# Performance work log

Hardware: AMD Instinct MI355X
Metric: run time of the kernel (lower is better)

## Reference

```python
import jax, jax.numpy as jnp
import numpy as np

EPS = 1e-5
NEG_SLOPE = 0.01  # torch F.leaky_relu default


def _batchnorm(h, gamma, beta):
    # BatchNorm1d in training mode: batch stats over node dim, biased variance
    mu = jnp.mean(h, axis=0)
    var = jnp.mean((h - mu) ** 2, axis=0)
    return gamma * (h - mu) * jax.lax.rsqrt(var + EPS) + beta


def setup_inputs() -> dict:
    N, E, H, ED = 16384, 524288, 128, 16
    key = jax.random.key(0)
    ks = jax.random.split(key, 12)
    s = 1.0 / np.sqrt(H)
    return {
        "x": jax.random.normal(ks[0], (N, H), jnp.float32),
        "edge_index": jax.random.randint(ks[1], (2, E), 0, N, jnp.int64),
        "edge_attr": jax.random.normal(ks[2], (E, ED), jnp.float32),
        "Wq": jax.random.normal(ks[3], (H, H), jnp.float32) * s,
        "bq": jnp.zeros((H,), jnp.float32),
        "Wk": jax.random.normal(ks[4], (H, H), jnp.float32) * s,
        "bk": jnp.zeros((H,), jnp.float32),
        "Wv": jax.random.normal(ks[5], (H, H), jnp.float32) * s,
        "bv": jnp.zeros((H,), jnp.float32),
        "We": jax.random.normal(ks[6], (ED, 1), jnp.float32) * (1.0 / np.sqrt(ED)),
        "be": jnp.zeros((1,), jnp.float32),
        "bn1_g": jnp.ones((H,), jnp.float32),
        "bn1_b": jnp.zeros((H,), jnp.float32),
        "W1": jax.random.normal(ks[7], (H, 2 * H), jnp.float32) * s,
        "b1": jnp.zeros((2 * H,), jnp.float32),
        "W2": jax.random.normal(ks[8], (2 * H, H), jnp.float32) * (1.0 / np.sqrt(2 * H)),
        "b2": jnp.zeros((H,), jnp.float32),
        "bn2_g": jnp.ones((H,), jnp.float32),
        "bn2_b": jnp.zeros((H,), jnp.float32),
    }


def reference(x, edge_index, edge_attr, Wq, bq, Wk, bk, Wv, bv, We, be,
              bn1_g, bn1_b, W1, b1, W2, b2, bn2_g, bn2_b):
    N = x.shape[0]
    Q = x @ Wq + bq  # [N, H]
    K = x @ Wk + bk
    V = x @ Wv + bv
    Ebias = (edge_attr @ We + be)[:, 0]  # [E], num_heads == 1
    src, dst = edge_index[0], edge_index[1]
    # per-edge dot product over the FULL hidden dim (as in the source)
    scores = jnp.sum(Q[src] * K[dst], axis=1) + Ebias  # [E]
    scores = jnp.where(scores >= 0, scores, NEG_SLOPE * scores)
    # to_dense_adj scatter-adds edge_attr into a dense [N, N] adjacency
    adj = jnp.zeros((N, N), x.dtype).at[src, dst].add(scores)
    attn = jax.nn.softmax(adj, axis=1)  # dense softmax incl. zero non-edges
    x_new = attn @ V  # [N, H]
    h = _batchnorm(x + x_new, bn1_g, bn1_b)
    ffn = jax.nn.relu(h @ W1 + b1) @ W2 + b2
    return _batchnorm(h + ffn, bn2_g, bn2_b)
```

## Files before the change

### kernel.cpp

```cpp
#include <hip/hip_runtime.h>
#include <hip/hip_bf16.h>
#include <math.h>

#define H 128
#define H2 256
#define SLAB 96
#define LDA 136
#define LDA2 264
#define EPS 1e-5f

typedef __attribute__((ext_vector_type(8))) short s16x8;
typedef __attribute__((ext_vector_type(4))) float f32x4;

__device__ __forceinline__ unsigned short f2bf(float f) {
  unsigned u = __float_as_uint(f);
  unsigned r = (u + 0x7FFFu + ((u >> 16) & 1u)) >> 16;
  return (unsigned short)r;
}
__device__ __forceinline__ float bf2f(unsigned short s) {
  return __uint_as_float(((unsigned)s) << 16);
}
__device__ __forceinline__ unsigned short f2h(float f) {
  union { unsigned short s; _Float16 h; } c; c.h = (_Float16)f; return c.s;
}
__device__ __forceinline__ float h2f(unsigned short u) {
  union { unsigned short s; _Float16 h; } c; c.s = u; return (float)c.h;
}

__global__ void wprep(const float* __restrict__ Wq, const float* __restrict__ Wk,
                      const float* __restrict__ Wv, const float* __restrict__ W1,
                      const float* __restrict__ W2,
                      short* qh, short* kh, short* vh, short* w1h, short* w2h,
                      int* __restrict__ cnt, float* __restrict__ stats, int N)
{
  int job = blockIdx.z;
  if (job == 5) {
    int t = blockIdx.x * 256 + threadIdx.x;
    if (t < N) cnt[t] = 0;
    if (t < 72 * H) stats[t] = 0.f;
    return;
  }
  const float* src; short* dh; int Kd, Nn; bool ashalf;
  if (job == 0)      { src = Wq; dh = qh;  Kd = 128; Nn = 128; ashalf = true; }
  else if (job == 1) { src = Wk; dh = kh;  Kd = 128; Nn = 128; ashalf = true; }
  else if (job == 2) { src = Wv; dh = vh;  Kd = 128; Nn = 128; ashalf = true; }
  else if (job == 3) { src = W1; dh = w1h; Kd = 128; Nn = 256; ashalf = false; }
  else               { src = W2; dh = w2h; Kd = 256; Nn = 128; ashalf = false; }
  int t = blockIdx.x * 256 + threadIdx.x;
  if (t >= Kd * Nn) return;
  int n = t / Kd, k = t - n * Kd;
  float v = src[(size_t)k * Nn + n];
  dh[t] = ashalf ? (short)f2h(v) : (short)f2bf(v);
}

__global__ __launch_bounds__(256) void qkv_mfma(
    const float* __restrict__ x,
    const short* __restrict__ Wqh, const short* __restrict__ Wkh,
    const short* __restrict__ Wvh,
    const float* __restrict__ bq, const float* __restrict__ bk,
    const float* __restrict__ bv,
    unsigned short* __restrict__ Qh, unsigned short* __restrict__ Kh,
    unsigned short* __restrict__ Vh, float* __restrict__ SVp,
    const float* __restrict__ ea, const float* __restrict__ We,
    const float* __restrict__ be, const int* __restrict__ ei,
    int* __restrict__ cnt, int2* __restrict__ slabDE,
    int E, int nqkv)
{
  __shared__ __align__(16) short A[64 * LDA];
  int tid = threadIdx.x;

  if (blockIdx.x >= nqkv) {
    int e = (blockIdx.x - nqkv) * 256 + tid;
    if (e < E) {
      float4 w0 = *(const float4*)&We[0], w1 = *(const float4*)&We[4];
      float4 w2 = *(const float4*)&We[8], w3 = *(const float4*)&We[12];
      const float4* p = (const float4*)&ea[(size_t)e * 16];
      float4 a0 = p[0], a1 = p[1], a2 = p[2], a3 = p[3];
      float s = a0.x * w0.x + a0.y * w0.y + a0.z * w0.z + a0.w * w0.w
              + a1.x * w1.x + a1.y * w1.y + a1.z * w1.z + a1.w * w1.w
              + a2.x * w2.x + a2.y * w2.y + a2.z * w2.z + a2.w * w2.w
              + a3.x * w3.x + a3.y * w3.y + a3.z * w3.z + a3.w * w3.w;
      s += be[0];
      int src = ei[e];
      int dst = ei[E + e];
      int pos = atomicAdd(&cnt[src], 1);
      if (pos < SLAB) {
        int2 rec; rec.x = dst; rec.y = __float_as_int(s);
        slabDE[(size_t)src * SLAB + pos] = rec;
      }
    }
    return;
  }

  int bm = blockIdx.x * 64;
  int wave = tid >> 6, lane = tid & 63;
  int quad = lane >> 4, l16 = lane & 15;
  int wn = wave * 32;

#pragma unroll
  for (int i = 0; i < 4; ++i) {
    int g = i * 256 + tid;
    int row = g >> 4, f = g & 15;
    const float4* xp = (const float4*)&x[(size_t)(bm + row) * H + f * 8];
    float4 v0 = xp[0], v1 = xp[1];
    float vv[8] = {v0.x, v0.y, v0.z, v0.w, v1.x, v1.y, v1.z, v1.w};
    s16x8 hv;
#pragma unroll
    for (int j = 0; j < 8; ++j) hv[j] = (short)f2h(vv[j]);
    *(s16x8*)&A[row * LDA + f * 8] = hv;
  }
  __syncthreads();

  for (int ph = 0; ph < 3; ++ph) {
    const short* Bh = (ph == 0) ? Wqh : (ph == 1) ? Wkh : Wvh;

    s16x8 bh[2][4];
#pragma unroll
    for (int nt = 0; nt < 2; ++nt)
#pragma unroll
      for (int ks = 0; ks < 4; ++ks)
        bh[nt][ks] = *(const s16x8*)&Bh[(size_t)(wn + nt * 16 + l16) * H + ks * 32 + quad * 8];

    f32x4 acc[4][2];
#pragma unroll
    for (int mt = 0; mt < 4; ++mt)
#pragma unroll
      for (int nt = 0; nt < 2; ++nt) acc[mt][nt] = (f32x4){0.f, 0.f, 0.f, 0.f};

#pragma unroll
    for (int ks = 0; ks < 4; ++ks) {
      int kof = ks * 32 + quad * 8;
      s16x8 ah[4];
#pragma unroll
      for (int mt = 0; mt < 4; ++mt)
        ah[mt] = *(s16x8*)&A[(mt * 16 + l16) * LDA + kof];
#pragma unroll
      for (int mt = 0; mt < 4; ++mt)
#pragma unroll
        for (int nt = 0; nt < 2; ++nt)
          acc[mt][nt] = __builtin_amdgcn_mfma_f32_16x16x32_f16(ah[mt], bh[nt][ks], acc[mt][nt], 0, 0, 0);
    }

    if (ph == 0) {
#pragma unroll
      for (int nt = 0; nt < 2; ++nt) {
        int col = wn + nt * 16 + l16;
        float bb = bq[col];
#pragma unroll
        for (int mt = 0; mt < 4; ++mt)
#pragma unroll
          for (int r = 0; r < 4; ++r) {
            int row = bm + mt * 16 + quad * 4 + r;
            Qh[(size_t)row * H + col] = f2h(acc[mt][nt][r] + bb);
          }
      }
    } else if (ph == 1) {
#pragma unroll
      for (int nt = 0; nt < 2; ++nt) {
        int col = wn + nt * 16 + l16;
        float bb = bk[col];
#pragma unroll
        for (int mt = 0; mt < 4; ++mt)
#pragma unroll
          for (int r = 0; r < 4; ++r) {
            int row = bm + mt * 16 + quad * 4 + r;
            Kh[(size_t)row * H + col] = f2h(acc[mt][nt][r] + bb);
          }
      }
    } else {
      int bank = blockIdx.x & 7;
#pragma unroll
      for (int nt = 0; nt < 2; ++nt) {
        int col = wn + nt * 16 + l16;
        float bb = bv[col];
        float ps = 0.f;
#pragma unroll
        for (int mt = 0; mt < 4; ++mt)
#pragma unroll
          for (int r = 0; r < 4; ++r) {
            int row = bm + mt * 16 + quad * 4 + r;
            float v = acc[mt][nt][r] + bb;
            Vh[(size_t)row * H + col] = f2h(v);
            ps += v;
          }
        ps += __shfl_xor(ps, 16);
        ps += __shfl_xor(ps, 32);
        if (quad == 0) atomicAdd(&SVp[bank * H + col], ps);
      }
    }
  }
}

__global__ __launch_bounds__(256) void attn_fused(
    const float* __restrict__ x,
    const unsigned short* __restrict__ Qh,
    const unsigned short* __restrict__ Kh,
    const unsigned short* __restrict__ Vh,
    const float* __restrict__ SVp, const int* __restrict__ cnt,
    const int2* __restrict__ slabDE,
    float* __restrict__ h1, float* __restrict__ sum1p, float* __restrict__ sq1p,
    int N)
{
  __shared__ float sv[4][SLAB];
  __shared__ int sd[4][SLAB];
  __shared__ short sown[4][SLAB];
  __shared__ int tab[4][128];
  __shared__ float csum[H], csq[H];
  int tid = threadIdx.x;
  int team = tid >> 6, lane = tid & 63;
  int i = blockIdx.x * 4 + team;
  int k = cnt[i]; if (k > SLAB) k = SLAB;
  size_t base = (size_t)i * SLAB;

  if (tid < H) { csum[tid] = 0.f; csq[tid] = 0.f; }
  tab[team][lane] = -1;
  tab[team][lane + 64] = -1;
  __syncthreads();

  for (int p = lane; p < k; p += 64) {
    int2 de = slabDE[base + p];
    sd[team][p] = de.x;
    sv[team][p] = __int_as_float(de.y);
  }

  float2 xx = *(const float2*)&x[(size_t)i * H + lane * 2];
  float sx = 0.f, sy = 0.f;
#pragma unroll
  for (int b = 0; b < 8; ++b) {
    float2 t = *(const float2*)&SVp[b * H + lane * 2];
    sx += t.x; sy += t.y;
  }

  int sub = lane & 7, slot = lane >> 3;
  const s16x8* qp = (const s16x8*)(Qh + (size_t)i * H);
  s16x8 qa = qp[sub], qb = qp[8 + sub];
  if (k > 0) {
    int c = 0;
    for (; c + 16 <= k; c += 16) {
      int p0 = c + slot, p1 = c + 8 + slot;
      int d0 = sd[team][p0], d1 = sd[team][p1];
      const s16x8* k0 = (const s16x8*)(Kh + (size_t)d0 * H);
      const s16x8* k1 = (const s16x8*)(Kh + (size_t)d1 * H);
      s16x8 ka0 = k0[sub], kb0 = k0[8 + sub];
      s16x8 ka1 = k1[sub], kb1 = k1[8 + sub];
      float s0 = 0.f, s1 = 0.f;
#pragma unroll
      for (int u = 0; u < 8; ++u) {
        s0 += h2f((unsigned short)qa[u]) * h2f((unsigned short)ka0[u]);
        s0 += h2f((unsigned short)qb[u]) * h2f((unsigned short)kb0[u]);
        s1 += h2f((unsigned short)qa[u]) * h2f((unsigned short)ka1[u]);
        s1 += h2f((unsigned short)qb[u]) * h2f((unsigned short)kb1[u]);
      }
      s0 += __shfl_xor(s0, 1); s1 += __shfl_xor(s1, 1);
      s0 += __shfl_xor(s0, 2); s1 += __shfl_xor(s1, 2);
      s0 += __shfl_xor(s0, 4); s1 += __shfl_xor(s1, 4);
      if (sub == 0) {
        float ss0 = s0 + sv[team][p0];
        sv[team][p0] = (ss0 >= 0.f) ? ss0 : 0.01f * ss0;
        float ss1 = s1 + sv[team][p1];
        sv[team][p1] = (ss1 >= 0.f) ? ss1 : 0.01f * ss1;
      }
    }
    for (; c < k; c += 8) {
      int p = c + slot;
      int pc = (p < k) ? p : 0;
      int d = sd[team][pc];
      const s16x8* kp = (const s16x8*)(Kh + (size_t)d * H);
      s16x8 ka = kp[sub], kb = kp[8 + sub];
      float s = 0.f;
#pragma unroll
      for (int u = 0; u < 8; ++u) {
        s += h2f((unsigned short)qa[u]) * h2f((unsigned short)ka[u]);
        s += h2f((unsigned short)qb[u]) * h2f((unsigned short)kb[u]);
      }
      s += __shfl_xor(s, 1);
      s += __shfl_xor(s, 2);
      s += __shfl_xor(s, 4);
      if (sub == 0 && p < k) {
        float ss = s + sv[team][p];
        sv[team][p] = (ss >= 0.f) ? ss : 0.01f * ss;
      }
    }
  }

  for (int p = lane; p < k; p += 64) {
    int d = sd[team][p];
    unsigned hsh = ((unsigned)d * 2654435761u) >> 25;
    int o;
    while (true) {
      int old = atomicCAS(&tab[team][hsh & 127], -1, p);
      if (old == -1) { o = p; break; }
      if (sd[team][old] == d) { o = old; break; }
      ++hsh;
    }
    sown[team][p] = (short)o;
  }
  for (int p = lane; p < k; p += 64) {
    int o = sown[team][p];
    if (o != p) atomicAdd(&sv[team][o], sv[team][p]);
  }

  float mx = 0.f;
  for (int p = lane; p < k; p += 64)
    if (sown[team][p] == (short)p) mx = fmaxf(mx, sv[team][p]);
#pragma unroll
  for (int msk = 32; msk; msk >>= 1) mx = fmaxf(mx, __shfl_xor(mx, msk));
  float em = __expf(-mx);

  float zl = 0.f;
  for (int p = lane; p < k; p += 64) {
    float cf = 0.f;
    if (sown[team][p] == (short)p) cf = __expf(sv[team][p] - mx) - em;
    sv[team][p] = cf;
    zl += cf;
  }
#pragma unroll
  for (int msk = 32; msk; msk >>= 1) zl += __shfl_xor(zl, msk);
  float Zi = 1.f / ((float)N * em + zl);

  const ushort2* V2 = (const ushort2*)Vh;
  float ax = em * sx, ay = em * sy;
  int c = 0;
  for (; c + 16 <= k; c += 16) {
    float cf[16]; int dd[16]; ushort2 vv[16];
#pragma unroll
    for (int u = 0; u < 16; ++u) { cf[u] = sv[team][c + u]; dd[u] = sd[team][c + u]; }
#pragma unroll
    for (int u = 0; u < 16; ++u) vv[u] = V2[(size_t)dd[u] * 64 + lane];
#pragma unroll
    for (int u = 0; u < 16; ++u) {
      ax += cf[u] * h2f(vv[u].x);
      ay += cf[u] * h2f(vv[u].y);
    }
  }
  for (; c + 8 <= k; c += 8) {
    float cf[8]; int dd[8]; ushort2 vv[8];
#pragma unroll
    for (int u = 0; u < 8; ++u) { cf[u] = sv[team][c + u]; dd[u] = sd[team][c + u]; }
#pragma unroll
    for (int u = 0; u < 8; ++u) vv[u] = V2[(size_t)dd[u] * 64 + lane];
#pragma unroll
    for (int u = 0; u < 8; ++u) {
      ax += cf[u] * h2f(vv[u].x);
      ay += cf[u] * h2f(vv[u].y);
    }
  }
  for (; c < k; ++c) {
    float cf = sv[team][c];
    ushort2 v0 = V2[(size_t)sd[team][c] * 64 + lane];
    ax += cf * h2f(v0.x); ay += cf * h2f(v0.y);
  }
  float ox = xx.x + ax * Zi;
  float oy = xx.y + ay * Zi;
  float2 ov; ov.x = ox; ov.y = oy;
  *(float2*)&h1[(size_t)i * H + lane * 2] = ov;

  int c0 = lane * 2;
  atomicAdd(&csum[c0 + 0], ox); atomicAdd(&csq[c0 + 0], ox * ox);
  atomicAdd(&csum[c0 + 1], oy); atomicAdd(&csq[c0 + 1], oy * oy);
  __syncthreads();
  if (tid < H) {
    int bank = blockIdx.x & 15;
    atomicAdd(&sum1p[bank * H + tid], csum[tid]);
    atomicAdd(&sq1p[bank * H + tid], csq[tid]);
  }
}

__global__ __launch_bounds__(256) void ffn_fused(
    const float* __restrict__ h1, const short* __restrict__ W1h,
    const float* __restrict__ b1, const short* __restrict__ W2h,
    const float* __restrict__ b2,
    const float* __restrict__ sum1p, const float* __restrict__ sq1p,
    const float* __restrict__ g1, const float* __restrict__ bb1,
    float* __restrict__ h2, float* __restrict__ sum2p, float* __restrict__ sq2p,
    float invN)
{
  __shared__ __align__(16) short As[32 * LDA];
  __shared__ __align__(16) short Ts[32 * LDA2];
  __shared__ float aF[H], bF[H];
  int tid = threadIdx.x;
  int bm = blockIdx.x * 32;
  int wave = tid >> 6, lane = tid & 63;
  int quad = lane >> 4, l16 = lane & 15;

  if (tid < H) {
    float s = 0.f, q = 0.f;
#pragma unroll
    for (int b = 0; b < 16; ++b) { s += sum1p[b * H + tid]; q += sq1p[b * H + tid]; }
    float mu = s * invN;
    float var = q * invN - mu * mu;
    float rs = rsqrtf(var + EPS);
    float a = g1[tid] * rs;
    aF[tid] = a;
    bF[tid] = bb1[tid] - a * mu;
  }
  __syncthreads();

  int f = tid & 15;
#pragma unroll
  for (int i = 0; i < 2; ++i) {
    int g = i * 256 + tid;
    int row = g >> 4;
    const float4* xp = (const float4*)&h1[(size_t)(bm + row) * H + f * 8];
    float4 v0 = xp[0], v1 = xp[1];
    float vv[8] = {v0.x, v0.y, v0.z, v0.w, v1.x, v1.y, v1.z, v1.w};
    s16x8 hv;
#pragma unroll
    for (int j = 0; j < 8; ++j) {
      int c = f * 8 + j;
      hv[j] = (short)f2bf(aF[c] * vv[j] + bF[c]);
    }
    *(s16x8*)&As[row * LDA + f * 8] = hv;
  }

  int wn1 = wave * 64;
  s16x8 b1f[4][4];
#pragma unroll
  for (int nt = 0; nt < 4; ++nt)
#pragma unroll
    for (int ks = 0; ks < 4; ++ks)
      b1f[nt][ks] = *(const s16x8*)&W1h[(size_t)(wn1 + nt * 16 + l16) * H + ks * 32 + quad * 8];
  __syncthreads();

  f32x4 acc1[2][4];
#pragma unroll
  for (int mt = 0; mt < 2; ++mt)
#pragma unroll
    for (int nt = 0; nt < 4; ++nt) acc1[mt][nt] = (f32x4){0.f, 0.f, 0.f, 0.f};

#pragma unroll
  for (int ks = 0; ks < 4; ++ks) {
    int kof = ks * 32 + quad * 8;
    s16x8 ah[2];
#pragma unroll
    for (int mt = 0; mt < 2; ++mt) ah[mt] = *(s16x8*)&As[(mt * 16 + l16) * LDA + kof];
#pragma unroll
    for (int mt = 0; mt < 2; ++mt)
#pragma unroll
      for (int nt = 0; nt < 4; ++nt)
        acc1[mt][nt] = __builtin_amdgcn_mfma_f32_16x16x32_bf16(ah[mt], b1f[nt][ks], acc1[mt][nt], 0, 0, 0);
  }

#pragma unroll
  for (int nt = 0; nt < 4; ++nt) {
    int col = wn1 + nt * 16 + l16;
    float bb = b1[col];
#pragma unroll
    for (int mt = 0; mt < 2; ++mt)
#pragma unroll
      for (int r = 0; r < 4; ++r) {
        int row = mt * 16 + quad * 4 + r;
        float v = acc1[mt][nt][r] + bb;
        v = v > 0.f ? v : 0.f;
        Ts[row * LDA2 + col] = (short)f2bf(v);
      }
  }

  int wn2 = wave * 32;
  s16x8 b2f[2][8];
#pragma unroll
  for (int nt = 0; nt < 2; ++nt)
#pragma unroll
    for (int ks = 0; ks < 8; ++ks)
      b2f[nt][ks] = *(const s16x8*)&W2h[(size_t)(wn2 + nt * 16 + l16) * H2 + ks * 32 + quad * 8];
  __syncthreads();

  f32x4 acc2[2][2];
#pragma unroll
  for (int mt = 0; mt < 2; ++mt)
#pragma unroll
    for (int nt = 0; nt < 2; ++nt) acc2[mt][nt] = (f32x4){0.f, 0.f, 0.f, 0.f};

#pragma unroll
  for (int ks = 0; ks < 8; ++ks) {
    int kof = ks * 32 + quad * 8;
    s16x8 ah[2];
#pragma unroll
    for (int mt = 0; mt < 2; ++mt) ah[mt] = *(s16x8*)&Ts[(mt * 16 + l16) * LDA2 + kof];
#pragma unroll
    for (int mt = 0; mt < 2; ++mt)
#pragma unroll
      for (int nt = 0; nt < 2; ++nt)
        acc2[mt][nt] = __builtin_amdgcn_mfma_f32_16x16x32_bf16(ah[mt], b2f[nt][ks], acc2[mt][nt], 0, 0, 0);
  }

  int bank = blockIdx.x & 15;
#pragma unroll
  for (int nt = 0; nt < 2; ++nt) {
    int col = wn2 + nt * 16 + l16;
    float ra = aF[col], rb = bF[col];
    float bb = b2[col];
    float ps = 0.f, pq = 0.f;
#pragma unroll
    for (int mt = 0; mt < 2; ++mt)
#pragma unroll
      for (int r = 0; r < 4; ++r) {
        int row = bm + mt * 16 + quad * 4 + r;
        float rr = ra * h1[(size_t)row * H + col] + rb;
        float v = acc2[mt][nt][r] + bb + rr;
        h2[(size_t)row * H + col] = v;
        ps += v; pq += v * v;
      }
    ps += __shfl_xor(ps, 16); ps += __shfl_xor(ps, 32);
    pq += __shfl_xor(pq, 16); pq += __shfl_xor(pq, 32);
    if (quad == 0) {
      atomicAdd(&sum2p[bank * H + col], ps);
      atomicAdd(&sq2p[bank * H + col], pq);
    }
  }
}

__global__ __launch_bounds__(256) void bn_apply(
    const float* __restrict__ X,
    const float* __restrict__ sum2p, const float* __restrict__ sq2p,
    const float* __restrict__ g2, const float* __restrict__ bb2,
    float* __restrict__ Y, size_t n4, float invN)
{
  __shared__ float A2s[H], B2s[H];
  int tid = threadIdx.x;
  if (tid < H) {
    float s = 0.f, q = 0.f;
#pragma unroll
    for (int b = 0; b < 16; ++b) { s += sum2p[b * H + tid]; q += sq2p[b * H + tid]; }
    float mu = s * invN;
    float var = q * invN - mu * mu;
    float rs = rsqrtf(var + EPS);
    float a = g2[tid] * rs;
    A2s[tid] = a;
    B2s[tid] = bb2[tid] - a * mu;
  }
  __syncthreads();
  size_t i = (size_t)blockIdx.x * blockDim.x + tid;
  if (i >= n4) return;
  float4 v = ((const float4*)X)[i];
  int c = (int)((i * 4) & (H - 1));
  float4 a = *(const float4*)&A2s[c];
  float4 b = *(const float4*)&B2s[c];
  v.x = a.x * v.x + b.x; v.y = a.y * v.y + b.y;
  v.z = a.z * v.z + b.z; v.w = a.w * v.w + b.w;
  ((float4*)Y)[i] = v;
}

extern "C" void kernel_launch(void* const* d_in, const int* in_sizes, int n_in,
                              void* d_out, int out_size, void* d_ws, size_t ws_size,
                              hipStream_t stream)
{
  const float* x  = (const float*)d_in[0];
  const int*   ei = (const int*)d_in[1];
  const float* ea = (const float*)d_in[2];
  const float* Wq = (const float*)d_in[3];
  const float* bq = (const float*)d_in[4];
  const float* Wk = (const float*)d_in[5];
  const float* bk = (const float*)d_in[6];
  const float* Wv = (const float*)d_in[7];
  const float* bv = (const float*)d_in[8];
  const float* We = (const float*)d_in[9];
  const float* be = (const float*)d_in[10];
  const float* g1 = (const float*)d_in[11];
  const float* bb1 = (const float*)d_in[12];
  const float* W1 = (const float*)d_in[13];
  const float* b1 = (const float*)d_in[14];
  const float* W2 = (const float*)d_in[15];
  const float* b2 = (const float*)d_in[16];
  const float* g2 = (const float*)d_in[17];
  const float* bb2 = (const float*)d_in[18];

  int N = in_sizes[0] / H;
  int E = in_sizes[2] / 16;
  size_t NH = (size_t)N * H;
  float invN = 1.0f / (float)N;

  unsigned short* Qh = (unsigned short*)d_ws;
  unsigned short* Kh = Qh + NH;
  unsigned short* Vh = Kh + NH;
  float* h1  = (float*)(Vh + NH);
  int2*  slabDE = (int2*)(h1 + NH);
  int*   cnt    = (int*)(slabDE + (size_t)N * SLAB);
  float* stats  = (float*)(cnt + N);
  float* SVp   = stats;
  float* sum1p = stats + 8 * H;
  float* sq1p  = sum1p + 16 * H;
  float* sum2p = sq1p + 16 * H;
  float* sq2p  = sum2p + 16 * H;
  float* statsEnd = sq2p + 16 * H;
  short* wbuf = (short*)statsEnd;
  short* Wqf = wbuf;
  short* Wkf = Wqf + 16384;
  short* Wvf = Wkf + 16384;
  short* W1h = Wvf + 16384;
  short* W2h = W1h + 32768;
  float* h2 = (float*)Qh;

  int nqkv = N / 64;
  int nscat = (E + 255) / 256;

  wprep<<<dim3(128, 1, 6), 256, 0, stream>>>(Wq, Wk, Wv, W1, W2,
      Wqf, Wkf, Wvf, W1h, W2h, cnt, stats, N);

  qkv_mfma<<<dim3(nqkv + nscat), 256, 0, stream>>>(
      x, Wqf, Wkf, Wvf, bq, bk, bv, Qh, Kh, Vh, SVp,
      ea, We, be, ei, cnt, slabDE, E, nqkv);

  attn_fused<<<dim3(N / 4), 256, 0, stream>>>(x, Qh, Kh, Vh, SVp, cnt, slabDE,
                                              h1, sum1p, sq1p, N);

  ffn_fused<<<dim3(N / 32), 256, 0, stream>>>(h1, W1h, b1, W2h, b2,
      sum1p, sq1p, g1, bb1, h2, sum2p, sq2p, invN);

  bn_apply<<<dim3((int)((NH / 4 + 255) / 256)), 256, 0, stream>>>(
      h2, sum2p, sq2p, g2, bb2, (float*)d_out, NH / 4, invN);
}
```

Baseline: 220.8 us.

## Bucket edges by 4-node groups with block-local counting before global atomics

The edge scatter now counts edges per 4-source-node bucket in shared memory and reserves space with one global atomic per bucket, writing packed (src,dst) records into 256-entry bucket slabs. The attention kernel reads its block's bucket once and splits edges to the four teams with shared atomics. The hash-based duplicate-destination table is replaced by a linear backward scan, the 16-wide V gather unroll is dropped, and the BN partial-sum banks grow from 16 to 64. The aim is fewer contended global atomics and a smaller edge buffer. The cost is a quadratic duplicate scan and possible silent truncation if a bucket exceeds 256 edges.

```diff
diff --git a/kernel.cpp b/kernel.cpp
--- a/kernel.cpp
+++ b/kernel.cpp
@@ -8,6 +8,8 @@
 #define LDA 136
 #define LDA2 264
 #define EPS 1e-5f
+#define NBK 4096
+#define BKC 256
 
 typedef __attribute__((ext_vector_type(8))) short s16x8;
 typedef __attribute__((ext_vector_type(4))) float f32x4;
@@ -31,13 +33,12 @@
                       const float* __restrict__ Wv, const float* __restrict__ W1,
                       const float* __restrict__ W2,
                       short* qh, short* kh, short* vh, short* w1h, short* w2h,
-                      int* __restrict__ cnt, float* __restrict__ stats, int N)
+                      float* __restrict__ stats, int N)
 {
   int job = blockIdx.z;
   if (job == 5) {
     int t = blockIdx.x * 256 + threadIdx.x;
-    if (t < N) cnt[t] = 0;
-    if (t < 72 * H) stats[t] = 0.f;
+    for (int s = t; s < 264 * H + NBK * 16; s += 32768) stats[s] = 0.f;
     return;
   }
   const float* src; short* dh; int Kd, Nn; bool ashalf;
@@ -63,30 +64,61 @@
     unsigned short* __restrict__ Vh, float* __restrict__ SVp,
     const float* __restrict__ ea, const float* __restrict__ We,
     const float* __restrict__ be, const int* __restrict__ ei,
-    int* __restrict__ cnt, int2* __restrict__ slabDE,
+    int* __restrict__ gcnt, int2* __restrict__ bedge,
     int E, int nqkv)
 {
   __shared__ __align__(16) short A[64 * LDA];
   int tid = threadIdx.x;
 
   if (blockIdx.x >= nqkv) {
-    int e = (blockIdx.x - nqkv) * 256 + tid;
-    if (e < E) {
-      float4 w0 = *(const float4*)&We[0], w1 = *(const float4*)&We[4];
-      float4 w2 = *(const float4*)&We[8], w3 = *(const float4*)&We[12];
-      const float4* p = (const float4*)&ea[(size_t)e * 16];
-      float4 a0 = p[0], a1 = p[1], a2 = p[2], a3 = p[3];
-      float s = a0.x * w0.x + a0.y * w0.y + a0.z * w0.z + a0.w * w0.w
-              + a1.x * w1.x + a1.y * w1.y + a1.z * w1.z + a1.w * w1.w
-              + a2.x * w2.x + a2.y * w2.y + a2.z * w2.z + a2.w * w2.w
-              + a3.x * w3.x + a3.y * w3.y + a3.z * w3.z + a3.w * w3.w;
-      s += be[0];
-      int src = ei[e];
-      int dst = ei[E + e];
-      int pos = atomicAdd(&cnt[src], 1);
-      if (pos < SLAB) {
-        int2 rec; rec.x = dst; rec.y = __float_as_int(s);
-        slabDE[(size_t)src * SLAB + pos] = rec;
+    int* lcnt = (int*)A;
+    int blk = blockIdx.x - nqkv;
+    int base = blk * 1024;
+    for (int s = tid; s < NBK; s += 256) lcnt[s] = 0;
+    __syncthreads();
+
+    float4 w0 = *(const float4*)&We[0], w1 = *(const float4*)&We[4];
+    float4 w2 = *(const float4*)&We[8], w3 = *(const float4*)&We[12];
+    float bias = be[0];
+
+    int bId[4], lpos[4], px[4]; float sc[4];
+#pragma unroll
+    for (int i = 0; i < 4; ++i) {
+      int e = base + i * 256 + tid;
+      bId[i] = -1;
+      if (e < E) {
+        const float4* p = (const float4*)&ea[(size_t)e * 16];
+        float4 a0 = p[0], a1 = p[1], a2 = p[2], a3 = p[3];
+        float s = a0.x * w0.x + a0.y * w0.y + a0.z * w0.z + a0.w * w0.w
+                + a1.x * w1.x + a1.y * w1.y + a1.z * w1.z + a1.w * w1.w
+                + a2.x * w2.x + a2.y * w2.y + a2.z * w2.z + a2.w * w2.w
+                + a3.x * w3.x + a3.y * w3.y + a3.z * w3.z + a3.w * w3.w;
+        s += bias;
+        int src = ei[e];
+        int dst = ei[E + e];
+        int b = src >> 2;
+        bId[i] = b;
+        px[i] = (src << 14) | dst;
+        sc[i] = s;
+        lpos[i] = atomicAdd(&lcnt[b], 1);
+      }
+    }
+    __syncthreads();
+#pragma unroll
+    for (int it = 0; it < NBK / 256; ++it) {
+      int s = it * 256 + tid;
+      int c = lcnt[s];
+      if (c > 0) lcnt[s] = atomicAdd(&gcnt[s * 16], c);
+    }
+    __syncthreads();
+#pragma unroll
+    for (int i = 0; i < 4; ++i) {
+      if (bId[i] >= 0) {
+        int pos = lcnt[bId[i]] + lpos[i];
+        if (pos < BKC) {
+          int2 rec; rec.x = px[i]; rec.y = __float_as_int(sc[i]);
+          bedge[(size_t)bId[i] * BKC + pos] = rec;
+        }
       }
     }
     return;
@@ -196,103 +228,102 @@
     const unsigned short* __restrict__ Qh,
     const unsigned short* __restrict__ Kh,
     const unsigned short* __restrict__ Vh,
-    const float* __restrict__ SVp, const int* __restrict__ cnt,
-    const int2* __restrict__ slabDE,
+    const float* __restrict__ SVp,
+    const int* __restrict__ gcnt, const int2* __restrict__ bedge,
     float* __restrict__ h1, float* __restrict__ sum1p, float* __restrict__ sq1p,
     int N)
 {
   __shared__ float sv[4][SLAB];
   __shared__ int sd[4][SLAB];
   __shared__ short sown[4][SLAB];
-  __shared__ int tab[4][128];
   __shared__ float csum[H], csq[H];
+  __shared__ int tcnt[4];
   int tid = threadIdx.x;
   int team = tid >> 6, lane = tid & 63;
-  int i = blockIdx.x * 4 + team;
-  int k = cnt[i]; if (k > SLAB) k = SLAB;
-  size_t base = (size_t)i * SLAB;
+  int b = blockIdx.x;
+  int i = b * 4 + team;
 
   if (tid < H) { csum[tid] = 0.f; csq[tid] = 0.f; }
-  tab[team][lane] = -1;
-  tab[team][lane + 64] = -1;
-  __syncthreads();
-
-  for (int p = lane; p < k; p += 64) {
-    int2 de = slabDE[base + p];
-    sd[team][p] = de.x;
-    sv[team][p] = __int_as_float(de.y);
-  }
+  if (tid < 4) tcnt[tid] = 0;
+  __syncthreads();
+
+  int m = gcnt[b * 16]; if (m > BKC) m = BKC;
+  const int2* bk = bedge + (size_t)b * BKC;
+  for (int r = tid; r < m; r += 256) {
+    int2 rec = bk[r];
+    int t = (rec.x >> 14) & 3;
+    int p = atomicAdd(&tcnt[t], 1);
+    if (p < SLAB) {
+      sd[t][p] = rec.x & 16383;
+      sv[t][p] = __int_as_float(rec.y);
+    }
+  }
+  __syncthreads();
+  int k = tcnt[team]; if (k > SLAB) k = SLAB;
 
   float2 xx = *(const float2*)&x[(size_t)i * H + lane * 2];
   float sx = 0.f, sy = 0.f;
 #pragma unroll
-  for (int b = 0; b < 8; ++b) {
-    float2 t = *(const float2*)&SVp[b * H + lane * 2];
+  for (int bb = 0; bb < 8; ++bb) {
+    float2 t = *(const float2*)&SVp[bb * H + lane * 2];
     sx += t.x; sy += t.y;
   }
 
   int sub = lane & 7, slot = lane >> 3;
   const s16x8* qp = (const s16x8*)(Qh + (size_t)i * H);
   s16x8 qa = qp[sub], qb = qp[8 + sub];
-  if (k > 0) {
-    int c = 0;
-    for (; c + 16 <= k; c += 16) {
-      int p0 = c + slot, p1 = c + 8 + slot;
-      int d0 = sd[team][p0], d1 = sd[team][p1];
-      const s16x8* k0 = (const s16x8*)(Kh + (size_t)d0 * H);
-      const s16x8* k1 = (const s16x8*)(Kh + (size_t)d1 * H);
-      s16x8 ka0 = k0[sub], kb0 = k0[8 + sub];
-      s16x8 ka1 = k1[sub], kb1 = k1[8 + sub];
-      float s0 = 0.f, s1 = 0.f;
-#pragma unroll
-      for (int u = 0; u < 8; ++u) {
-        s0 += h2f((unsigned short)qa[u]) * h2f((unsigned short)ka0[u]);
-        s0 += h2f((unsigned short)qb[u]) * h2f((unsigned short)kb0[u]);
-        s1 += h2f((unsigned short)qa[u]) * h2f((unsigned short)ka1[u]);
-        s1 += h2f((unsigned short)qb[u]) * h2f((unsigned short)kb1[u]);
-      }
-      s0 += __shfl_xor(s0, 1); s1 += __shfl_xor(s1, 1);
-      s0 += __shfl_xor(s0, 2); s1 += __shfl_xor(s1, 2);
-      s0 += __shfl_xor(s0, 4); s1 += __shfl_xor(s1, 4);
-      if (sub == 0) {
-        float ss0 = s0 + sv[team][p0];
-        sv[team][p0] = (ss0 >= 0.f) ? ss0 : 0.01f * ss0;
-        float ss1 = s1 + sv[team][p1];
-        sv[team][p1] = (ss1 >= 0.f) ? ss1 : 0.01f * ss1;
-      }
-    }
-    for (; c < k; c += 8) {
-      int p = c + slot;
-      int pc = (p < k) ? p : 0;
-      int d = sd[team][pc];
-      const s16x8* kp = (const s16x8*)(Kh + (size_t)d * H);
-      s16x8 ka = kp[sub], kb = kp[8 + sub];
-      float s = 0.f;
-#pragma unroll
-      for (int u = 0; u < 8; ++u) {
-        s += h2f((unsigned short)qa[u]) * h2f((unsigned short)ka[u]);
-        s += h2f((unsigned short)qb[u]) * h2f((unsigned short)kb[u]);
-      }
-      s += __shfl_xor(s, 1);
-      s += __shfl_xor(s, 2);
-      s += __shfl_xor(s, 4);
-      if (sub == 0 && p < k) {
-        float ss = s + sv[team][p];
-        sv[team][p] = (ss >= 0.f) ? ss : 0.01f * ss;
-      }
+  int c = 0;
+  for (; c + 16 <= k; c += 16) {
+    int p0 = c + slot, p1 = c + 8 + slot;
+    int d0 = sd[team][p0], d1 = sd[team][p1];
+    const s16x8* k0 = (const s16x8*)(Kh + (size_t)d0 * H);
+    const s16x8* k1 = (const s16x8*)(Kh + (size_t)d1 * H);
+    s16x8 ka0 = k0[sub], kb0 = k0[8 + sub];
+    s16x8 ka1 = k1[sub], kb1 = k1[8 + sub];
+    float s0 = 0.f, s1 = 0.f;
+#pragma unroll
+    for (int u = 0; u < 8; ++u) {
+      s0 += h2f((unsigned short)qa[u]) * h2f((unsigned short)ka0[u]);
+      s0 += h2f((unsigned short)qb[u]) * h2f((unsigned short)kb0[u]);
+      s1 += h2f((unsigned short)qa[u]) * h2f((unsigned short)ka1[u]);
+      s1 += h2f((unsigned short)qb[u]) * h2f((unsigned short)kb1[u]);
+    }
+    s0 += __shfl_xor(s0, 1); s1 += __shfl_xor(s1, 1);
+    s0 += __shfl_xor(s0, 2); s1 += __shfl_xor(s1, 2);
+    s0 += __shfl_xor(s0, 4); s1 += __shfl_xor(s1, 4);
+    if (sub == 0) {
+      float ss0 = s0 + sv[team][p0];
+      sv[team][p0] = (ss0 >= 0.f) ? ss0 : 0.01f * ss0;
+      float ss1 = s1 + sv[team][p1];
+      sv[team][p1] = (ss1 >= 0.f) ? ss1 : 0.01f * ss1;
+    }
+  }
+  for (; c < k; c += 8) {
+    int p = c + slot;
+    int pc = (p < k) ? p : 0;
+    int d = sd[team][pc];
+    const s16x8* kp = (const s16x8*)(Kh + (size_t)d * H);
+    s16x8 ka = kp[sub], kb = kp[8 + sub];
+    float s = 0.f;
+#pragma unroll
+    for (int u = 0; u < 8; ++u) {
+      s += h2f((unsigned short)qa[u]) * h2f((unsigned short)ka[u]);
+      s += h2f((unsigned short)qb[u]) * h2f((unsigned short)kb[u]);
+    }
+    s += __shfl_xor(s, 1);
+    s += __shfl_xor(s, 2);
+    s += __shfl_xor(s, 4);
+    if (sub == 0 && p < k) {
+      float ss = s + sv[team][p];
+      sv[team][p] = (ss >= 0.f) ? ss : 0.01f * ss;
     }
   }
 
   for (int p = lane; p < k; p += 64) {
     int d = sd[team][p];
-    unsigned hsh = ((unsigned)d * 2654435761u) >> 25;
-    int o;
-    while (true) {
-      int old = atomicCAS(&tab[team][hsh & 127], -1, p);
-      if (old == -1) { o = p; break; }
-      if (sd[team][old] == d) { o = old; break; }
-      ++hsh;
-    }
+    int o = p;
+    for (int q = p - 1; q >= 0; --q)
+      o = (sd[team][q] == d) ? q : o;
     sown[team][p] = (short)o;
   }
   for (int p = lane; p < k; p += 64) {
@@ -320,19 +351,7 @@
 
   const ushort2* V2 = (const ushort2*)Vh;
   float ax = em * sx, ay = em * sy;
-  int c = 0;
-  for (; c + 16 <= k; c += 16) {
-    float cf[16]; int dd[16]; ushort2 vv[16];
-#pragma unroll
-    for (int u = 0; u < 16; ++u) { cf[u] = sv[team][c + u]; dd[u] = sd[team][c + u]; }
-#pragma unroll
-    for (int u = 0; u < 16; ++u) vv[u] = V2[(size_t)dd[u] * 64 + lane];
-#pragma unroll
-    for (int u = 0; u < 16; ++u) {
-      ax += cf[u] * h2f(vv[u].x);
-      ay += cf[u] * h2f(vv[u].y);
-    }
-  }
+  c = 0;
   for (; c + 8 <= k; c += 8) {
     float cf[8]; int dd[8]; ushort2 vv[8];
 #pragma unroll
@@ -360,7 +379,7 @@
   atomicAdd(&csum[c0 + 1], oy); atomicAdd(&csq[c0 + 1], oy * oy);
   __syncthreads();
   if (tid < H) {
-    int bank = blockIdx.x & 15;
+    int bank = blockIdx.x & 63;
     atomicAdd(&sum1p[bank * H + tid], csum[tid]);
     atomicAdd(&sq1p[bank * H + tid], csq[tid]);
   }
@@ -386,7 +405,7 @@
   if (tid < H) {
     float s = 0.f, q = 0.f;
 #pragma unroll
-    for (int b = 0; b < 16; ++b) { s += sum1p[b * H + tid]; q += sq1p[b * H + tid]; }
+    for (int b = 0; b < 64; ++b) { s += sum1p[b * H + tid]; q += sq1p[b * H + tid]; }
     float mu = s * invN;
     float var = q * invN - mu * mu;
     float rs = rsqrtf(var + EPS);
@@ -484,7 +503,7 @@
         acc2[mt][nt] = __builtin_amdgcn_mfma_f32_16x16x32_bf16(ah[mt], b2f[nt][ks], acc2[mt][nt], 0, 0, 0);
   }
 
-  int bank = blockIdx.x & 15;
+  int bank = blockIdx.x & 63;
 #pragma unroll
   for (int nt = 0; nt < 2; ++nt) {
     int col = wn2 + nt * 16 + l16;
@@ -521,7 +540,7 @@
   if (tid < H) {
     float s = 0.f, q = 0.f;
 #pragma unroll
-    for (int b = 0; b < 16; ++b) { s += sum2p[b * H + tid]; q += sq2p[b * H + tid]; }
+    for (int b = 0; b < 64; ++b) { s += sum2p[b * H + tid]; q += sq2p[b * H + tid]; }
     float mu = s * invN;
     float var = q * invN - mu * mu;
     float rs = rsqrtf(var + EPS);
@@ -574,35 +593,34 @@
   unsigned short* Kh = Qh + NH;
   unsigned short* Vh = Kh + NH;
   float* h1  = (float*)(Vh + NH);
-  int2*  slabDE = (int2*)(h1 + NH);
-  int*   cnt    = (int*)(slabDE + (size_t)N * SLAB);
-  float* stats  = (float*)(cnt + N);
+  float* stats = h1 + NH;
   float* SVp   = stats;
   float* sum1p = stats + 8 * H;
-  float* sq1p  = sum1p + 16 * H;
-  float* sum2p = sq1p + 16 * H;
-  float* sq2p  = sum2p + 16 * H;
-  float* statsEnd = sq2p + 16 * H;
-  short* wbuf = (short*)statsEnd;
+  float* sq1p  = sum1p + 64 * H;
+  float* sum2p = sq1p + 64 * H;
+  float* sq2p  = sum2p + 64 * H;
+  int*   gcnt  = (int*)(sq2p + 64 * H);
+  short* wbuf = (short*)(gcnt + NBK * 16);
   short* Wqf = wbuf;
   short* Wkf = Wqf + 16384;
   short* Wvf = Wkf + 16384;
   short* W1h = Wvf + 16384;
   short* W2h = W1h + 32768;
+  int2*  bedge = (int2*)(W2h + 32768);
   float* h2 = (float*)Qh;
 
   int nqkv = N / 64;
-  int nscat = (E + 255) / 256;
+  int nscat = (E + 1023) / 1024;
 
   wprep<<<dim3(128, 1, 6), 256, 0, stream>>>(Wq, Wk, Wv, W1, W2,
-      Wqf, Wkf, Wvf, W1h, W2h, cnt, stats, N);
+      Wqf, Wkf, Wvf, W1h, W2h, stats, N);
 
   qkv_mfma<<<dim3(nqkv + nscat), 256, 0, stream>>>(
       x, Wqf, Wkf, Wvf, bq, bk, bv, Qh, Kh, Vh, SVp,
-      ea, We, be, ei, cnt, slabDE, E, nqkv);
-
-  attn_fused<<<dim3(N / 4), 256, 0, stream>>>(x, Qh, Kh, Vh, SVp, cnt, slabDE,
-                                              h1, sum1p, sq1p, N);
+      ea, We, be, ei, gcnt, bedge, E, nqkv);
+
+  attn_fused<<<dim3(NBK), 256, 0, stream>>>(x, Qh, Kh, Vh, SVp, gcnt, bedge,
+                                            h1, sum1p, sq1p, N);
 
   ffn_fused<<<dim3(N / 32), 256, 0, stream>>>(h1, W1h, b1, W2h, b2,
       sum1p, sq1p, g1, bb1, h2, sum2p, sq2p, invN);
```

New measurement: 221.3 us. Within noise of the previous version (+0.2%).
